# Optimization experiments

Hardware: AMD Instinct MI355X
Metric: run time of the kernel (lower is better)

Reference implementation:

```python
import jax, jax.numpy as jnp
import numpy as np

N = 10000   # nodes
E = 160000  # edges
D = 128     # input feature dim
C = 128     # embedding_channels
K = 4       # top-k neighbors


def gcn_conv(x, edge_index, W, b, n):
    """PyG-style GCNConv: sym-normalized aggregation with self loops."""
    h = x @ W  # [n, C]
    ar = jnp.arange(n)
    row = jnp.concatenate([edge_index[0], ar])
    col = jnp.concatenate([edge_index[1], ar])
    deg = jax.ops.segment_sum(jnp.ones_like(row, dtype=h.dtype), row, num_segments=n)
    dinv = jax.lax.rsqrt(jnp.maximum(deg, 1e-12))
    norm = dinv[row] * dinv[col]            # [E+n]
    msg = h[col] * norm[:, None]            # gather + scale
    out = jax.ops.segment_sum(msg, row, num_segments=n)
    return out + b


def sample_without_replacement(x, temperature, q, k):
    n = x.shape[0]
    sq = jnp.sum(x * x, axis=1)
    # squared pairwise distances == cdist(x,x)**2
    d2 = jnp.maximum(sq[:, None] + sq[None, :] - 2.0 * (x @ x.T), 0.0)  # [n, n]
    logprobs = -temperature * d2
    gumbel = -jnp.log(-jnp.log(q + 1e-8))   # q ~ U(0,1), matches rand_like + 1e-8
    lq = logprobs + gumbel
    vals, idx = jax.lax.top_k(lq, k)        # [n, k]
    rows = jnp.repeat(jnp.arange(n), k)
    edges = jnp.stack([idx.reshape(-1), rows])  # [2, n*k]
    return edges, vals


def fix_self_loops(edges, n):
    # original fix_self_loops discards the remove result and just appends self loops
    ar = jnp.arange(n)
    return jnp.concatenate([edges, jnp.stack([ar, ar])], axis=1)


def setup_inputs() -> dict:
    key = jax.random.key(0)
    k1, k2, k3, k4 = jax.random.split(key, 4)
    x = jax.random.normal(k1, (N, D), dtype=jnp.float32)
    edge_index = jax.random.randint(k2, (2, E), 0, N, dtype=jnp.int64)
    q = jax.random.uniform(k3, (N, N), dtype=jnp.float32)
    W = jax.random.normal(k4, (D, C), dtype=jnp.float32) / np.sqrt(D)
    b = jnp.zeros((C,), dtype=jnp.float32)
    temperature = jnp.asarray(4.0, dtype=jnp.float32)
    return {"x": x, "edge_index": edge_index, "q": q, "W": W, "b": b,
            "temperature": temperature}


def reference(x, edge_index, q, W, b, temperature):
    n = x.shape[0]
    h = gcn_conv(x, edge_index, W, b, n)
    edge_index_hat, logprobs = sample_without_replacement(h, temperature, q, K)
    edge_index_hat = fix_self_loops(edge_index_hat, n)
    return h, edge_index_hat, logprobs
```

## Files before the change

### kernel.cpp

```cpp
#include <hip/hip_runtime.h>

#define NN 10000
#define NPAD 10112
#define EE 160000
#define DD 128
#define KT 4

constexpr int JSPLIT = 16;
constexpr int ITILES = 157;
constexpr int JCHUNK = 628;
constexpr double FPSCALE = 1099511627776.0;
constexpr float NEG_INF = -3.402823466e38f;
constexpr float NLN2 = -0.69314718055994531f;

constexpr int RSTRIDE_B = 272;
constexpr int LO_OFF = 64 * RSTRIDE_B;

typedef __attribute__((ext_vector_type(8))) short short8;
typedef __attribute__((ext_vector_type(8))) unsigned short ushort8;
typedef __attribute__((ext_vector_type(4))) float f32x4;

__device__ inline unsigned short bf_rn(float x) {
    unsigned u = __float_as_uint(x);
    unsigned r = (u + 0x7fffu + ((u >> 16) & 1u)) >> 16;
    return (unsigned short)r;
}
__device__ inline float bf_f(unsigned short h) {
    return __uint_as_float(((unsigned)h) << 16);
}

__global__ __launch_bounds__(256) void k_gemm(const float* __restrict__ x,
                                              const float* __restrict__ W,
                                              float* __restrict__ hpre) {
    __shared__ float4 Ws4[128 * 32];
    __shared__ float4 xs4[32 * 32];
    const int t = threadIdx.x;
    const int r0 = blockIdx.x * 32;
    const float4* W4 = reinterpret_cast<const float4*>(W);
    const float4* x4 = reinterpret_cast<const float4*>(x);
#pragma unroll
    for (int i = 0; i < 16; ++i) Ws4[i * 256 + t] = W4[i * 256 + t];
#pragma unroll
    for (int i = 0; i < 4; ++i) {
        int f = i * 256 + t;
        int g = r0 * 32 + f;
        xs4[f] = (g < NN * 32) ? x4[g] : make_float4(0.f, 0.f, 0.f, 0.f);
    }
    __syncthreads();
    const int c = t & 31;
    const int rg = t >> 5;
    float4 acc[4] = {};
    for (int k4 = 0; k4 < 32; ++k4) {
        float4 w0 = Ws4[(k4 * 4 + 0) * 32 + c];
        float4 w1 = Ws4[(k4 * 4 + 1) * 32 + c];
        float4 w2 = Ws4[(k4 * 4 + 2) * 32 + c];
        float4 w3 = Ws4[(k4 * 4 + 3) * 32 + c];
#pragma unroll
        for (int r = 0; r < 4; ++r) {
            float4 xv = xs4[(rg * 4 + r) * 32 + k4];
            acc[r].x = fmaf(xv.w, w3.x, fmaf(xv.z, w2.x, fmaf(xv.y, w1.x, fmaf(xv.x, w0.x, acc[r].x))));
            acc[r].y = fmaf(xv.w, w3.y, fmaf(xv.z, w2.y, fmaf(xv.y, w1.y, fmaf(xv.x, w0.y, acc[r].y))));
            acc[r].z = fmaf(xv.w, w3.z, fmaf(xv.z, w2.z, fmaf(xv.y, w1.z, fmaf(xv.x, w0.z, acc[r].z))));
            acc[r].w = fmaf(xv.w, w3.w, fmaf(xv.z, w2.w, fmaf(xv.y, w1.w, fmaf(xv.x, w0.w, acc[r].w))));
        }
    }
#pragma unroll
    for (int r = 0; r < 4; ++r) {
        int row = r0 + rg * 4 + r;
        if (row < NN) reinterpret_cast<float4*>(hpre)[row * 32 + c] = acc[r];
    }
}

__global__ void k_count(const int* __restrict__ ei, int* __restrict__ cnt) {
    int e = blockIdx.x * blockDim.x + threadIdx.x;
    if (e < EE) atomicAdd(&cnt[ei[e]], 1);
}

__global__ void k_scan(int* __restrict__ cnt, int* __restrict__ rowptr,
                       float* __restrict__ dinv) {
    __shared__ int part[1024];
    int t = threadIdx.x;
    int base = t * 10;
    int loc[10];
    int s = 0;
#pragma unroll
    for (int k = 0; k < 10; ++k) {
        int idx = base + k;
        int v = (idx < NN) ? cnt[idx] : 0;
        loc[k] = s; s += v;
    }
    part[t] = s;
    __syncthreads();
    for (int off = 1; off < 1024; off <<= 1) {
        int v = (t >= off) ? part[t - off] : 0;
        __syncthreads();
        part[t] += v;
        __syncthreads();
    }
    int pre = (t > 0) ? part[t - 1] : 0;
#pragma unroll
    for (int k = 0; k < 10; ++k) {
        int idx = base + k;
        if (idx < NN) {
            rowptr[idx] = pre + loc[k];
            int d = cnt[idx];
            dinv[idx] = 1.0f / sqrtf((float)(d + 1));
            cnt[idx] = 0;
        }
    }
    if (t == 1023) rowptr[NN] = part[1023];
}

__global__ void k_fill(const int* __restrict__ ei, const int* __restrict__ rowptr,
                       int* __restrict__ wcnt, int* __restrict__ csr) {
    int e = blockIdx.x * blockDim.x + threadIdx.x;
    if (e >= EE) return;
    int r = ei[e];
    int pos = atomicAdd(&wcnt[r], 1);
    csr[rowptr[r] + pos] = ei[EE + e];
}

__global__ void k_gather(const float* __restrict__ hpre, const int* __restrict__ rowptr,
                         const int* __restrict__ csr, const float* __restrict__ dinv,
                         const float* __restrict__ b, float* __restrict__ out,
                         unsigned short* __restrict__ hhi, unsigned short* __restrict__ hlo,
                         float* __restrict__ sqout) {
    int r = blockIdx.x;
    int t = threadIdx.x;
    __shared__ float part[2];
    float outv = 0.f;
    if (r < NN) {
        float dr = dinv[r];
        float v0 = hpre[r * DD + t] * dr * dr;
        long long acc = llrint((double)v0 * FPSCALE);
        int s = rowptr[r], e = rowptr[r + 1];
        for (int k = s; k < e; ++k) {
            int c = csr[k];
            float w = dr * dinv[c];
            float p = hpre[c * DD + t] * w;
            acc += llrint((double)p * FPSCALE);
        }
        outv = (float)((double)acc * (1.0 / FPSCALE)) + b[t];
        out[r * DD + t] = outv;
    }
    unsigned short h0 = bf_rn(outv);
    float rs = outv - bf_f(h0);
    unsigned short l0 = bf_rn(rs);
    hhi[r * DD + t] = h0;
    hlo[r * DD + t] = l0;
    float s2 = outv * outv;
#pragma unroll
    for (int off = 32; off; off >>= 1) s2 += __shfl_xor(s2, off, 64);
    if ((t & 63) == 0) part[t >> 6] = s2;
    __syncthreads();
    if (t == 0) sqout[r] = part[0] + part[1];
}

#define BETTER(v1, j1, v2, j2) ((v1) > (v2) || ((v1) == (v2) && (j1) < (j2)))

#define INSERT4(tvv, tjj, v, j)                                               \
    if (BETTER(v, j, tvv[3], tjj[3])) {                                       \
        tvv[3] = v; tjj[3] = j;                                               \
        _Pragma("unroll")                                                     \
        for (int rr = 3; rr > 0; --rr) {                                      \
            if (BETTER(tvv[rr], tjj[rr], tvv[rr - 1], tjj[rr - 1])) {         \
                float t0 = tvv[rr]; tvv[rr] = tvv[rr - 1]; tvv[rr - 1] = t0;  \
                int t1 = tjj[rr]; tjj[rr] = tjj[rr - 1]; tjj[rr - 1] = t1;    \
            }                                                                 \
        }                                                                     \
    }

__global__ __launch_bounds__(256, 4) void k_topk(
    const unsigned short* __restrict__ hhi, const unsigned short* __restrict__ hlo,
    const float* __restrict__ sq, const float* __restrict__ q,
    const float* __restrict__ tptr, float* __restrict__ pvals, int* __restrict__ pidx) {
    __shared__ __align__(16) unsigned short Bsh[2 * 64 * 136];
    __shared__ __align__(16) float sqs[64];

    const int blk = blockIdx.x;
    const int itile = blk >> 4;
    const int split = blk & 15;
    const int ibase = itile * 64;
    const int jstart = split * JCHUNK;
    const int jlimit = min(NN, jstart + JCHUNK);
    const float T = *tptr;

    const int tid = threadIdx.x;
    const int w = tid >> 6;
    const int lane = tid & 63;
    const int n = lane & 15;
    const int kl = lane >> 4;
    const int kl4 = kl * 4;

    short8 ihi[4], ilo[4];
    {
        int ra = ibase + 16 * w + n;
        const unsigned short* pa = hhi + ra * DD + kl * 8;
        const unsigned short* pl = hlo + ra * DD + kl * 8;
#pragma unroll
        for (int ks = 0; ks < 4; ++ks) {
            ihi[ks] = *reinterpret_cast<const short8*>(pa + ks * 32);
            ilo[ks] = *reinterpret_cast<const short8*>(pl + ks * 32);
        }
    }

    const int i_glob = ibase + 16 * w + n;
    const int ic = min(i_glob, NN - 1);
    const float sqi = sq[ic];
    const float* qrow = q + (size_t)ic * NN;

    char* wp = (char*)Bsh + (tid >> 4) * RSTRIDE_B + (tid & 15) * 16;
    const char* rp = (const char*)Bsh + n * RSTRIDE_B + kl * 16;
    const char* sp = (const char*)sqs + kl * 16;

    float tv[4];
    int tj[4];
#pragma unroll
    for (int s = 0; s < 4; ++s) { tv[s] = NEG_INF; tj[s] = 0x7fffffff; }

    for (int jt = 0; jt < 10; ++jt) {
        const int jbase = jstart + jt * 64;
        __syncthreads();
        {
            const unsigned short* gh = hhi + (size_t)(jbase + (tid >> 4)) * DD + (tid & 15) * 8;
            const unsigned short* gl = hlo + (size_t)(jbase + (tid >> 4)) * DD + (tid & 15) * 8;
#pragma unroll
            for (int p = 0; p < 4; ++p) {
                *reinterpret_cast<ushort8*>(wp + p * (16 * RSTRIDE_B)) =
                    *reinterpret_cast<const ushort8*>(gh + p * 2048);
                *reinterpret_cast<ushort8*>(wp + LO_OFF + p * (16 * RSTRIDE_B)) =
                    *reinterpret_cast<const ushort8*>(gl + p * 2048);
            }
        }

        float4 qv[4];
        if (jbase <= NN - 64) {
            const float* qt = qrow + (jbase + kl4);
#pragma unroll
            for (int jf = 0; jf < 4; ++jf)
                qv[jf] = *reinterpret_cast<const float4*>(qt + 16 * jf);
        } else {
#pragma unroll
            for (int jf = 0; jf < 4; ++jf) {
                int j0 = jbase + 16 * jf + kl4;
                int jq = min(j0, NN - 4);
                qv[jf] = *reinterpret_cast<const float4*>(qrow + jq);
            }
        }

        if (tid < 64) sqs[tid] = sq[jbase + tid];
        __syncthreads();

#pragma unroll
        for (int jf = 0; jf < 4; ++jf) {
            short8 jh[4], jl[4];
#pragma unroll
            for (int ks = 0; ks < 4; ++ks) {
                jh[ks] = *reinterpret_cast<const short8*>(rp + jf * (16 * RSTRIDE_B) + ks * 64);
                jl[ks] = *reinterpret_cast<const short8*>(rp + LO_OFF + jf * (16 * RSTRIDE_B) + ks * 64);
            }
            f32x4 acc = {0.f, 0.f, 0.f, 0.f};
#pragma unroll
            for (int ks = 0; ks < 4; ++ks)
                acc = __builtin_amdgcn_mfma_f32_16x16x32_bf16(jh[ks], ihi[ks], acc, 0, 0, 0);
#pragma unroll
            for (int ks = 0; ks < 4; ++ks)
                acc = __builtin_amdgcn_mfma_f32_16x16x32_bf16(jl[ks], ihi[ks], acc, 0, 0, 0);
#pragma unroll
            for (int ks = 0; ks < 4; ++ks)
                acc = __builtin_amdgcn_mfma_f32_16x16x32_bf16(jh[ks], ilo[ks], acc, 0, 0, 0);

            const float4 sq4 = *reinterpret_cast<const float4*>(sp + jf * 64);
            const int j0 = jbase + 16 * jf + kl4;
            const float* sqp = reinterpret_cast<const float*>(&sq4);
            const float* qp = reinterpret_cast<const float*>(&qv[jf]);
#pragma unroll
            for (int r = 0; r < 4; ++r) {
                float d2 = fmaxf(fmaf(-2.f, acc[r], sqi + sqp[r]), 0.f);
                float qe = qp[r] + 1e-8f;
                float t  = (qe - 1.f) * __builtin_amdgcn_rcpf(qe + 1.f);
                float t2 = t * t;
                float pp = fmaf(0.11111111f, t2, 0.14285714f);
                pp = fmaf(pp, t2, 0.2f);
                pp = fmaf(pp, t2, 0.33333333f);
                pp = fmaf(pp, t2, 1.f);
                float udir = (-2.f * t) * pp;
                float ulog = __log2f(qe) * NLN2;
                float u = (qe >= 0.5f) ? udir : ulog;
                float g = __log2f(u) * NLN2;
                float v = fmaf(-T, d2, g);
                if (jt == 9) {
                    if (j0 + r >= jlimit) v = NEG_INF;
                }
                if (v > tv[3]) {
                    int j = j0 + r;
                    tv[3] = v; tj[3] = j;
#pragma unroll
                    for (int rr = 3; rr > 0; --rr) {
                        if (BETTER(tv[rr], tj[rr], tv[rr - 1], tj[rr - 1])) {
                            float t0 = tv[rr]; tv[rr] = tv[rr - 1]; tv[rr - 1] = t0;
                            int t1 = tj[rr]; tj[rr] = tj[rr - 1]; tj[rr - 1] = t1;
                        }
                    }
                }
            }
        }
    }

    __syncthreads();
    float* mv = reinterpret_cast<float*>(Bsh);
    int* mj = reinterpret_cast<int*>((char*)Bsh + LO_OFF);
    {
        int rl = 16 * w + n;
#pragma unroll
        for (int s = 0; s < 4; ++s) {
            mv[rl * 16 + kl4 + s] = tv[s];
            mj[rl * 16 + kl4 + s] = tj[s];
        }
    }
    __syncthreads();
    if (tid < 64) {
        int i = ibase + tid;
        float bv[4] = {NEG_INF, NEG_INF, NEG_INF, NEG_INF};
        int bj[4] = {0x7fffffff, 0x7fffffff, 0x7fffffff, 0x7fffffff};
        for (int c = 0; c < 16; ++c) {
            float v = mv[tid * 16 + c];
            int j = mj[tid * 16 + c];
            INSERT4(bv, bj, v, j)
        }
        if (i < NN) {
#pragma unroll
            for (int s = 0; s < 4; ++s) {
                pvals[(split * NN + i) * 4 + s] = bv[s];
                pidx[(split * NN + i) * 4 + s] = bj[s];
            }
        }
    }
}

__global__ void k_merge(const float* __restrict__ pvals, const int* __restrict__ pidx,
                        float* __restrict__ out) {
    int i = blockIdx.x * blockDim.x + threadIdx.x;
    if (i >= NN) return;
    float mv[4] = {NEG_INF, NEG_INF, NEG_INF, NEG_INF};
    int mj[4] = {0x7fffffff, 0x7fffffff, 0x7fffffff, 0x7fffffff};
    for (int s = 0; s < JSPLIT; ++s) {
#pragma unroll
        for (int r = 0; r < 4; ++r) {
            float v = pvals[(s * NN + i) * 4 + r];
            int j = pidx[(s * NN + i) * 4 + r];
            INSERT4(mv, mj, v, j)
        }
    }
    float* eidx = out + NN * DD;
    float* erow = eidx + (NN * KT + NN);
    float* lp = erow + (NN * KT + NN);
#pragma unroll
    for (int r = 0; r < 4; ++r) {
        eidx[i * 4 + r] = (float)mj[r];
        erow[i * 4 + r] = (float)i;
        lp[i * 4 + r] = mv[r];
    }
    eidx[NN * KT + i] = (float)i;
    erow[NN * KT + i] = (float)i;
}

extern "C" void kernel_launch(void* const* d_in, const int* in_sizes, int n_in,
                              void* d_out, int out_size, void* d_ws, size_t ws_size,
                              hipStream_t stream) {
    const float* x = (const float*)d_in[0];
    const int* ei = (const int*)d_in[1];
    const float* q = (const float*)d_in[2];
    const float* W = (const float*)d_in[3];
    const float* b = (const float*)d_in[4];
    const float* temp = (const float*)d_in[5];
    float* out = (float*)d_out;

    char* ws = (char*)d_ws;
    float* hpre = (float*)(ws + 0);
    unsigned short* hhi = (unsigned short*)(ws + 5120000);
    unsigned short* hlo = (unsigned short*)(ws + 7708672);
    float* pvals = (float*)(ws + 10297344);
    int* pidx = (int*)(ws + 12857344);
    float* sq = (float*)(ws + 15417344);
    int* cnt = (int*)(ws + 15457792);
    int* rowptr = (int*)(ws + 15497792);
    float* dinv = (float*)(ws + 15537808);
    int* csr = (int*)(ws + 15577808);

    hipMemsetAsync(cnt, 0, 40000, stream);

    k_gemm<<<313, 256, 0, stream>>>(x, W, hpre);
    k_count<<<(EE + 255) / 256, 256, 0, stream>>>(ei, cnt);
    k_scan<<<1, 1024, 0, stream>>>(cnt, rowptr, dinv);
    k_fill<<<(EE + 255) / 256, 256, 0, stream>>>(ei, rowptr, cnt, csr);
    k_gather<<<NPAD, 128, 0, stream>>>(hpre, rowptr, csr, dinv, b, out, hhi, hlo, sq);
    k_topk<<<ITILES * JSPLIT, 256, 0, stream>>>(hhi, hlo, sq, q, temp, pvals, pidx);
    k_merge<<<(NN + 255) / 256, 256, 0, stream>>>(pvals, pidx, out);
}
```

Measured before the change: 362.3 us.

## Process two 64-row i-tiles per block to reuse staged j tiles

Doubles the top-k block's row tile from 64 to 128, so each wave keeps two sets of i-row fragments in registers and runs two MFMA accumulator chains against the same j tile held in LDS. This halves the global-to-LDS staging and LDS reads of the j-side embeddings per computed distance, and halves the number of blocks. The cost is higher register pressure: the occupancy hint drops from 4 to 3 blocks per CU, and the grid has fewer blocks to spread across CUs. The Gumbel and top-k insert work per element is unchanged.

```diff
diff --git a/kernel.cpp b/kernel.cpp
--- a/kernel.cpp
+++ b/kernel.cpp
@@ -7,7 +7,8 @@
 #define KT 4
 
 constexpr int JSPLIT = 16;
-constexpr int ITILES = 157;
+constexpr int BM = 128;
+constexpr int ITILES = 79;
 constexpr int JCHUNK = 628;
 constexpr double FPSCALE = 1099511627776.0;
 constexpr float NEG_INF = -3.402823466e38f;
@@ -170,7 +171,19 @@
         }                                                                     \
     }
 
-__global__ __launch_bounds__(256, 4) void k_topk(
+#define GATED_INSERT(tvv, tjj, v, j)                                          \
+    if ((v) > tvv[3]) {                                                       \
+        tvv[3] = (v); tjj[3] = (j);                                           \
+        _Pragma("unroll")                                                     \
+        for (int rr = 3; rr > 0; --rr) {                                      \
+            if (BETTER(tvv[rr], tjj[rr], tvv[rr - 1], tjj[rr - 1])) {         \
+                float t0 = tvv[rr]; tvv[rr] = tvv[rr - 1]; tvv[rr - 1] = t0;  \
+                int t1 = tjj[rr]; tjj[rr] = tjj[rr - 1]; tjj[rr - 1] = t1;    \
+            }                                                                 \
+        }                                                                     \
+    }
+
+__global__ __launch_bounds__(256, 3) void k_topk(
     const unsigned short* __restrict__ hhi, const unsigned short* __restrict__ hlo,
     const float* __restrict__ sq, const float* __restrict__ q,
     const float* __restrict__ tptr, float* __restrict__ pvals, int* __restrict__ pidx) {
@@ -180,7 +193,7 @@
     const int blk = blockIdx.x;
     const int itile = blk >> 4;
     const int split = blk & 15;
-    const int ibase = itile * 64;
+    const int ibase = itile * BM;
     const int jstart = split * JCHUNK;
     const int jlimit = min(NN, jstart + JCHUNK);
     const float T = *tptr;
@@ -192,31 +205,44 @@
     const int kl = lane >> 4;
     const int kl4 = kl * 4;
 
-    short8 ihi[4], ilo[4];
+    short8 ihi0[4], ilo0[4], ihi1[4], ilo1[4];
     {
-        int ra = ibase + 16 * w + n;
-        const unsigned short* pa = hhi + ra * DD + kl * 8;
-        const unsigned short* pl = hlo + ra * DD + kl * 8;
+        int ra0 = ibase + 16 * w + n;
+        int ra1 = ra0 + 64;
+        const unsigned short* pa0 = hhi + ra0 * DD + kl * 8;
+        const unsigned short* pl0 = hlo + ra0 * DD + kl * 8;
+        const unsigned short* pa1 = hhi + ra1 * DD + kl * 8;
+        const unsigned short* pl1 = hlo + ra1 * DD + kl * 8;
 #pragma unroll
         for (int ks = 0; ks < 4; ++ks) {
-            ihi[ks] = *reinterpret_cast<const short8*>(pa + ks * 32);
-            ilo[ks] = *reinterpret_cast<const short8*>(pl + ks * 32);
-        }
-    }
-
-    const int i_glob = ibase + 16 * w + n;
-    const int ic = min(i_glob, NN - 1);
-    const float sqi = sq[ic];
-    const float* qrow = q + (size_t)ic * NN;
+            ihi0[ks] = *reinterpret_cast<const short8*>(pa0 + ks * 32);
+            ilo0[ks] = *reinterpret_cast<const short8*>(pl0 + ks * 32);
+            ihi1[ks] = *reinterpret_cast<const short8*>(pa1 + ks * 32);
+            ilo1[ks] = *reinterpret_cast<const short8*>(pl1 + ks * 32);
+        }
+    }
+
+    float sqi[2];
+    const float* qrow[2];
+#pragma unroll
+    for (int s = 0; s < 2; ++s) {
+        int i = ibase + 16 * w + n + 64 * s;
+        int ic = min(i, NN - 1);
+        sqi[s] = sq[ic];
+        qrow[s] = q + (size_t)ic * NN;
+    }
 
     char* wp = (char*)Bsh + (tid >> 4) * RSTRIDE_B + (tid & 15) * 16;
     const char* rp = (const char*)Bsh + n * RSTRIDE_B + kl * 16;
     const char* sp = (const char*)sqs + kl * 16;
 
-    float tv[4];
-    int tj[4];
-#pragma unroll
-    for (int s = 0; s < 4; ++s) { tv[s] = NEG_INF; tj[s] = 0x7fffffff; }
+    float tv0[4], tv1[4];
+    int tj0[4], tj1[4];
+#pragma unroll
+    for (int s = 0; s < 4; ++s) {
+        tv0[s] = NEG_INF; tj0[s] = 0x7fffffff;
+        tv1[s] = NEG_INF; tj1[s] = 0x7fffffff;
+    }
 
     for (int jt = 0; jt < 10; ++jt) {
         const int jbase = jstart + jt * 64;
@@ -233,18 +259,22 @@
             }
         }
 
-        float4 qv[4];
+        float4 qv0[4], qv1[4];
         if (jbase <= NN - 64) {
-            const float* qt = qrow + (jbase + kl4);
-#pragma unroll
-            for (int jf = 0; jf < 4; ++jf)
-                qv[jf] = *reinterpret_cast<const float4*>(qt + 16 * jf);
+            const float* qt0 = qrow[0] + (jbase + kl4);
+            const float* qt1 = qrow[1] + (jbase + kl4);
+#pragma unroll
+            for (int jf = 0; jf < 4; ++jf) {
+                qv0[jf] = *reinterpret_cast<const float4*>(qt0 + 16 * jf);
+                qv1[jf] = *reinterpret_cast<const float4*>(qt1 + 16 * jf);
+            }
         } else {
 #pragma unroll
             for (int jf = 0; jf < 4; ++jf) {
                 int j0 = jbase + 16 * jf + kl4;
                 int jq = min(j0, NN - 4);
-                qv[jf] = *reinterpret_cast<const float4*>(qrow + jq);
+                qv0[jf] = *reinterpret_cast<const float4*>(qrow[0] + jq);
+                qv1[jf] = *reinterpret_cast<const float4*>(qrow[1] + jq);
             }
         }
 
@@ -259,49 +289,66 @@
                 jh[ks] = *reinterpret_cast<const short8*>(rp + jf * (16 * RSTRIDE_B) + ks * 64);
                 jl[ks] = *reinterpret_cast<const short8*>(rp + LO_OFF + jf * (16 * RSTRIDE_B) + ks * 64);
             }
-            f32x4 acc = {0.f, 0.f, 0.f, 0.f};
-#pragma unroll
-            for (int ks = 0; ks < 4; ++ks)
-                acc = __builtin_amdgcn_mfma_f32_16x16x32_bf16(jh[ks], ihi[ks], acc, 0, 0, 0);
-#pragma unroll
-            for (int ks = 0; ks < 4; ++ks)
-                acc = __builtin_amdgcn_mfma_f32_16x16x32_bf16(jl[ks], ihi[ks], acc, 0, 0, 0);
-#pragma unroll
-            for (int ks = 0; ks < 4; ++ks)
-                acc = __builtin_amdgcn_mfma_f32_16x16x32_bf16(jh[ks], ilo[ks], acc, 0, 0, 0);
+            f32x4 acc0 = {0.f, 0.f, 0.f, 0.f};
+            f32x4 acc1 = {0.f, 0.f, 0.f, 0.f};
+#pragma unroll
+            for (int ks = 0; ks < 4; ++ks) {
+                acc0 = __builtin_amdgcn_mfma_f32_16x16x32_bf16(jh[ks], ihi0[ks], acc0, 0, 0, 0);
+                acc1 = __builtin_amdgcn_mfma_f32_16x16x32_bf16(jh[ks], ihi1[ks], acc1, 0, 0, 0);
+            }
+#pragma unroll
+            for (int ks = 0; ks < 4; ++ks) {
+                acc0 = __builtin_amdgcn_mfma_f32_16x16x32_bf16(jl[ks], ihi0[ks], acc0, 0, 0, 0);
+                acc1 = __builtin_amdgcn_mfma_f32_16x16x32_bf16(jl[ks], ihi1[ks], acc1, 0, 0, 0);
+            }
+#pragma unroll
+            for (int ks = 0; ks < 4; ++ks) {
+                acc0 = __builtin_amdgcn_mfma_f32_16x16x32_bf16(jh[ks], ilo0[ks], acc0, 0, 0, 0);
+                acc1 = __builtin_amdgcn_mfma_f32_16x16x32_bf16(jh[ks], ilo1[ks], acc1, 0, 0, 0);
+            }
 
             const float4 sq4 = *reinterpret_cast<const float4*>(sp + jf * 64);
             const int j0 = jbase + 16 * jf + kl4;
             const float* sqp = reinterpret_cast<const float*>(&sq4);
-            const float* qp = reinterpret_cast<const float*>(&qv[jf]);
+            const float* qp0 = reinterpret_cast<const float*>(&qv0[jf]);
+            const float* qp1 = reinterpret_cast<const float*>(&qv1[jf]);
 #pragma unroll
             for (int r = 0; r < 4; ++r) {
-                float d2 = fmaxf(fmaf(-2.f, acc[r], sqi + sqp[r]), 0.f);
-                float qe = qp[r] + 1e-8f;
-                float t  = (qe - 1.f) * __builtin_amdgcn_rcpf(qe + 1.f);
-                float t2 = t * t;
-                float pp = fmaf(0.11111111f, t2, 0.14285714f);
-                pp = fmaf(pp, t2, 0.2f);
-                pp = fmaf(pp, t2, 0.33333333f);
-                pp = fmaf(pp, t2, 1.f);
-                float udir = (-2.f * t) * pp;
-                float ulog = __log2f(qe) * NLN2;
-                float u = (qe >= 0.5f) ? udir : ulog;
-                float g = __log2f(u) * NLN2;
-                float v = fmaf(-T, d2, g);
-                if (jt == 9) {
-                    if (j0 + r >= jlimit) v = NEG_INF;
+                const int j = j0 + r;
+                const bool oob = (jt == 9) && (j >= jlimit);
+                {
+                    float d2 = fmaxf(fmaf(-2.f, acc0[r], sqi[0] + sqp[r]), 0.f);
+                    float qe = qp0[r] + 1e-8f;
+                    float t  = (qe - 1.f) * __builtin_amdgcn_rcpf(qe + 1.f);
+                    float t2 = t * t;
+                    float pp = fmaf(0.11111111f, t2, 0.14285714f);
+                    pp = fmaf(pp, t2, 0.2f);
+                    pp = fmaf(pp, t2, 0.33333333f);
+                    pp = fmaf(pp, t2, 1.f);
+                    float udir = (-2.f * t) * pp;
+                    float ulog = __log2f(qe) * NLN2;
+                    float u = (qe >= 0.5f) ? udir : ulog;
+                    float g = __log2f(u) * NLN2;
+                    float v = fmaf(-T, d2, g);
+                    if (oob) v = NEG_INF;
+                    GATED_INSERT(tv0, tj0, v, j)
                 }
-                if (v > tv[3]) {
-                    int j = j0 + r;
-                    tv[3] = v; tj[3] = j;
-#pragma unroll
-                    for (int rr = 3; rr > 0; --rr) {
-                        if (BETTER(tv[rr], tj[rr], tv[rr - 1], tj[rr - 1])) {
-                            float t0 = tv[rr]; tv[rr] = tv[rr - 1]; tv[rr - 1] = t0;
-                            int t1 = tj[rr]; tj[rr] = tj[rr - 1]; tj[rr - 1] = t1;
-                        }
-                    }
+                {
+                    float d2 = fmaxf(fmaf(-2.f, acc1[r], sqi[1] + sqp[r]), 0.f);
+                    float qe = qp1[r] + 1e-8f;
+                    float t  = (qe - 1.f) * __builtin_amdgcn_rcpf(qe + 1.f);
+                    float t2 = t * t;
+                    float pp = fmaf(0.11111111f, t2, 0.14285714f);
+                    pp = fmaf(pp, t2, 0.2f);
+                    pp = fmaf(pp, t2, 0.33333333f);
+                    pp = fmaf(pp, t2, 1.f);
+                    float udir = (-2.f * t) * pp;
+                    float ulog = __log2f(qe) * NLN2;
+                    float u = (qe >= 0.5f) ? udir : ulog;
+                    float g = __log2f(u) * NLN2;
+                    float v = fmaf(-T, d2, g);
+                    if (oob) v = NEG_INF;
+                    GATED_INSERT(tv1, tj1, v, j)
                 }
             }
         }
@@ -311,15 +358,18 @@
     float* mv = reinterpret_cast<float*>(Bsh);
     int* mj = reinterpret_cast<int*>((char*)Bsh + LO_OFF);
     {
-        int rl = 16 * w + n;
+        int rl0 = 16 * w + n;
+        int rl1 = rl0 + 64;
 #pragma unroll
         for (int s = 0; s < 4; ++s) {
-            mv[rl * 16 + kl4 + s] = tv[s];
-            mj[rl * 16 + kl4 + s] = tj[s];
+            mv[rl0 * 16 + kl4 + s] = tv0[s];
+            mj[rl0 * 16 + kl4 + s] = tj0[s];
+            mv[rl1 * 16 + kl4 + s] = tv1[s];
+            mj[rl1 * 16 + kl4 + s] = tj1[s];
         }
     }
     __syncthreads();
-    if (tid < 64) {
+    if (tid < BM) {
         int i = ibase + tid;
         float bv[4] = {NEG_INF, NEG_INF, NEG_INF, NEG_INF};
         int bj[4] = {0x7fffffff, 0x7fffffff, 0x7fffffff, 0x7fffffff};
```

Measured after the change: 453.2 us. 25.1% more time.

## Load top-k B fragments directly from global memory instead of staging in LDS

Applied to the files above, without the earlier changes.

The top-k kernel no longer copies each 64-row tile of the hi/lo bf16 embeddings, plus the squared norms, into shared memory between barriers. Each wave now reads its MFMA B fragments and squared norms straight from global memory, relying on the L1/L2 caches for reuse across the four waves. This removes two block-wide barriers per tile and most of the LDS footprint, and the min-blocks launch-bound hint is dropped. In exchange, global/cache traffic for B roughly quadruples, and the fragment reads are less coalesced than the staged copy was.

```diff
diff --git a/kernel.cpp b/kernel.cpp
--- a/kernel.cpp
+++ b/kernel.cpp
@@ -12,9 +12,6 @@
 constexpr double FPSCALE = 1099511627776.0;
 constexpr float NEG_INF = -3.402823466e38f;
 constexpr float NLN2 = -0.69314718055994531f;
-
-constexpr int RSTRIDE_B = 272;
-constexpr int LO_OFF = 64 * RSTRIDE_B;
 
 typedef __attribute__((ext_vector_type(8))) short short8;
 typedef __attribute__((ext_vector_type(8))) unsigned short ushort8;
@@ -170,12 +167,12 @@
         }                                                                     \
     }
 
-__global__ __launch_bounds__(256, 4) void k_topk(
+__global__ __launch_bounds__(256) void k_topk(
     const unsigned short* __restrict__ hhi, const unsigned short* __restrict__ hlo,
     const float* __restrict__ sq, const float* __restrict__ q,
     const float* __restrict__ tptr, float* __restrict__ pvals, int* __restrict__ pidx) {
-    __shared__ __align__(16) unsigned short Bsh[2 * 64 * 136];
-    __shared__ __align__(16) float sqs[64];
+    __shared__ float mvs[64 * 16];
+    __shared__ int   mjs[64 * 16];
 
     const int blk = blockIdx.x;
     const int itile = blk >> 4;
@@ -195,8 +192,8 @@
     short8 ihi[4], ilo[4];
     {
         int ra = ibase + 16 * w + n;
-        const unsigned short* pa = hhi + ra * DD + kl * 8;
-        const unsigned short* pl = hlo + ra * DD + kl * 8;
+        const unsigned short* pa = hhi + (size_t)ra * DD + kl * 8;
+        const unsigned short* pl = hlo + (size_t)ra * DD + kl * 8;
 #pragma unroll
         for (int ks = 0; ks < 4; ++ks) {
             ihi[ks] = *reinterpret_cast<const short8*>(pa + ks * 32);
@@ -209,9 +206,8 @@
     const float sqi = sq[ic];
     const float* qrow = q + (size_t)ic * NN;
 
-    char* wp = (char*)Bsh + (tid >> 4) * RSTRIDE_B + (tid & 15) * 16;
-    const char* rp = (const char*)Bsh + n * RSTRIDE_B + kl * 16;
-    const char* sp = (const char*)sqs + kl * 16;
+    const unsigned short* jbh = hhi + (size_t)(jstart + n) * DD + kl * 8;
+    const unsigned short* jbl = hlo + (size_t)(jstart + n) * DD + kl * 8;
 
     float tv[4];
     int tj[4];
@@ -220,18 +216,6 @@
 
     for (int jt = 0; jt < 10; ++jt) {
         const int jbase = jstart + jt * 64;
-        __syncthreads();
-        {
-            const unsigned short* gh = hhi + (size_t)(jbase + (tid >> 4)) * DD + (tid & 15) * 8;
-            const unsigned short* gl = hlo + (size_t)(jbase + (tid >> 4)) * DD + (tid & 15) * 8;
-#pragma unroll
-            for (int p = 0; p < 4; ++p) {
-                *reinterpret_cast<ushort8*>(wp + p * (16 * RSTRIDE_B)) =
-                    *reinterpret_cast<const ushort8*>(gh + p * 2048);
-                *reinterpret_cast<ushort8*>(wp + LO_OFF + p * (16 * RSTRIDE_B)) =
-                    *reinterpret_cast<const ushort8*>(gl + p * 2048);
-            }
-        }
 
         float4 qv[4];
         if (jbase <= NN - 64) {
@@ -248,16 +232,16 @@
             }
         }
 
-        if (tid < 64) sqs[tid] = sq[jbase + tid];
-        __syncthreads();
+        const unsigned short* th = jbh + (size_t)jt * (64 * DD);
+        const unsigned short* tl = jbl + (size_t)jt * (64 * DD);
 
 #pragma unroll
         for (int jf = 0; jf < 4; ++jf) {
             short8 jh[4], jl[4];
 #pragma unroll
             for (int ks = 0; ks < 4; ++ks) {
-                jh[ks] = *reinterpret_cast<const short8*>(rp + jf * (16 * RSTRIDE_B) + ks * 64);
-                jl[ks] = *reinterpret_cast<const short8*>(rp + LO_OFF + jf * (16 * RSTRIDE_B) + ks * 64);
+                jh[ks] = *reinterpret_cast<const short8*>(th + jf * (16 * DD) + ks * 32);
+                jl[ks] = *reinterpret_cast<const short8*>(tl + jf * (16 * DD) + ks * 32);
             }
             f32x4 acc = {0.f, 0.f, 0.f, 0.f};
 #pragma unroll
@@ -270,8 +254,8 @@
             for (int ks = 0; ks < 4; ++ks)
                 acc = __builtin_amdgcn_mfma_f32_16x16x32_bf16(jh[ks], ilo[ks], acc, 0, 0, 0);
 
-            const float4 sq4 = *reinterpret_cast<const float4*>(sp + jf * 64);
             const int j0 = jbase + 16 * jf + kl4;
+            const float4 sq4 = *reinterpret_cast<const float4*>(sq + j0);
             const float* sqp = reinterpret_cast<const float*>(&sq4);
             const float* qp = reinterpret_cast<const float*>(&qv[jf]);
 #pragma unroll
@@ -307,15 +291,12 @@
         }
     }
 
-    __syncthreads();
-    float* mv = reinterpret_cast<float*>(Bsh);
-    int* mj = reinterpret_cast<int*>((char*)Bsh + LO_OFF);
     {
         int rl = 16 * w + n;
 #pragma unroll
         for (int s = 0; s < 4; ++s) {
-            mv[rl * 16 + kl4 + s] = tv[s];
-            mj[rl * 16 + kl4 + s] = tj[s];
+            mvs[rl * 16 + kl4 + s] = tv[s];
+            mjs[rl * 16 + kl4 + s] = tj[s];
         }
     }
     __syncthreads();
@@ -324,8 +305,8 @@
         float bv[4] = {NEG_INF, NEG_INF, NEG_INF, NEG_INF};
         int bj[4] = {0x7fffffff, 0x7fffffff, 0x7fffffff, 0x7fffffff};
         for (int c = 0; c < 16; ++c) {
-            float v = mv[tid * 16 + c];
-            int j = mj[tid * 16 + c];
+            float v = mvs[tid * 16 + c];
+            int j = mjs[tid * 16 + c];
             INSERT4(bv, bj, v, j)
         }
         if (i < NN) {
```

New measurement: 565.5 us. 1.56x slower.
